# Performance work log

Hardware: AMD Instinct MI355X
Metric: run time of the kernel (lower is better)

Reference implementation:

```python
import jax, jax.numpy as jnp
import numpy as np

WD, WH, WW = 2, 7, 7
N = WD * WH * WW          # 98 tokens per window
DIM = 128
HEADS = 4
HEAD_DIM = DIM // HEADS   # 32
B_ = 2048                 # num_windows * batch
NW = 64                   # windows per image (mask leading dim)
TABLE = (2 * WD - 1) * (2 * WH - 1) * (2 * WW - 1)  # 507


def _relative_position_index():
    coords = np.stack(np.meshgrid(np.arange(WD), np.arange(WH), np.arange(WW), indexing='ij'))
    flat = coords.reshape(3, -1)                     # [3, N]
    rel = flat[:, :, None] - flat[:, None, :]        # [3, N, N]
    rel = rel.transpose(1, 2, 0).copy()              # [N, N, 3]
    rel[:, :, 0] += WD - 1
    rel[:, :, 1] += WH - 1
    rel[:, :, 2] += WW - 1
    rel[:, :, 0] *= (2 * WH - 1) * (2 * WW - 1)
    rel[:, :, 1] *= 2 * WW - 1
    return rel.sum(-1).astype(np.int32)             # [N, N]


def setup_inputs() -> dict:
    key = jax.random.key(0)
    ks = jax.random.split(key, 6)
    x = jax.random.normal(ks[0], (B_, N, DIM), dtype=jnp.float32)
    mask = jax.random.normal(ks[1], (NW, N, N), dtype=jnp.float32)
    qkv_w = jax.random.normal(ks[2], (3 * DIM, DIM), dtype=jnp.float32) * 0.02
    qkv_b = jnp.zeros((3 * DIM,), dtype=jnp.float32)
    proj_w = jax.random.normal(ks[3], (DIM, DIM), dtype=jnp.float32) * 0.02
    proj_b = jnp.zeros((DIM,), dtype=jnp.float32)
    bias_table = jax.random.normal(ks[4], (TABLE, HEADS), dtype=jnp.float32) * 0.02
    rel_idx = jnp.asarray(_relative_position_index())
    return {"x": x, "mask": mask, "qkv_w": qkv_w, "qkv_b": qkv_b,
            "proj_w": proj_w, "proj_b": proj_b, "bias_table": bias_table,
            "rel_idx": rel_idx}


def reference(x, mask, qkv_w, qkv_b, proj_w, proj_b, bias_table, rel_idx):
    b, n, c = x.shape
    hd = c // HEADS
    scale = hd ** -0.5
    qkv = x @ qkv_w.T + qkv_b                          # [B_, N, 3C]
    qkv = qkv.reshape(b, n, 3, HEADS, hd)
    qkv = jnp.transpose(qkv, (2, 0, 3, 1, 4))          # [3, B_, H, N, hd]
    q, k, v = qkv[0], qkv[1], qkv[2]
    attn = jnp.einsum('bhnd,bhmd->bhnm', q * scale, k)  # [B_, H, N, N]
    # gathered relative position bias
    bias = bias_table[rel_idx.reshape(-1)].reshape(n, n, HEADS)
    bias = jnp.transpose(bias, (2, 0, 1))               # [H, N, N]
    attn = attn + bias[None]
    nw = mask.shape[0]
    attn = attn.reshape(b // nw, nw, HEADS, n, n) + mask[None, :, None]
    attn = jax.nn.softmax(attn.reshape(b, HEADS, n, n), axis=-1)
    out = jnp.einsum('bhnm,bhmd->bnhd', attn, v).reshape(b, n, c)
    out = out @ proj_w.T + proj_b
    return out
```

## Files before the change

kernel.cpp:

```cpp
#include <hip/hip_runtime.h>
#include <stdint.h>

#define NTOK 98
#define DIM 128
#define HEADS 4
#define HD 32
#define BWIN 2048
#define NW 64
#define SCALE 0.17677669529663687f
#define QSTR 40
#define VSTR 104

typedef __bf16 bf16_t;
typedef bf16_t bf16x8 __attribute__((ext_vector_type(8)));
typedef float f32x4 __attribute__((ext_vector_type(4)));
typedef unsigned short u16;
typedef unsigned int u32;
typedef unsigned long long u64;

__device__ __forceinline__ u16 f2bf(float f) {
    union { bf16_t h; u16 u; } v; v.h = (bf16_t)f; return v.u;
}
__device__ __forceinline__ float bf2f(u16 b) {
    union { u16 u; bf16_t h; } v; v.u = b; return (float)v.h;
}

__global__ void k0_prep(const float* __restrict__ qkv_w, const float* __restrict__ proj_w,
                        const float* __restrict__ mask,
                        const float* __restrict__ bias_table, const int* __restrict__ rel_idx,
                        u16* __restrict__ qkvw_bf, u16* __restrict__ pw_bf,
                        u16* __restrict__ mbT)
{
    int t = blockIdx.x * 256 + threadIdx.x;
    if (t < 49152) {
        qkvw_bf[t] = f2bf(qkv_w[t]);
    } else if (t < 65536) {
        int r = t - 49152;
        pw_bf[r] = f2bf(proj_w[r]);
    } else {
        int r = t - 65536;
        int w    = r / 50176;
        int rem  = r - w * 50176;
        int hh   = rem / 12544;
        int rem2 = rem - hh * 12544;
        int i    = rem2 >> 7;
        int c    = rem2 & 127;
        int l16  = c >> 3;
        int njp  = c & 7;
        int j    = njp * 16 + l16;
        float val = 0.f;
        if (njp < 7 && j < NTOK)
            val = mask[w * 9604 + i * NTOK + j] + bias_table[rel_idx[i * NTOK + j] * HEADS + hh];
        mbT[r] = f2bf(val);
    }
}

__global__ __launch_bounds__(256, 4) void k_attn(
    const float* __restrict__ x, const u16* __restrict__ qkvw_bf,
    const float* __restrict__ qkv_b, const u16* __restrict__ mbT,
    u16* __restrict__ OG)
{
    __shared__ __align__(16) u16 qL[NTOK * QSTR];
    __shared__ __align__(16) u16 kL[NTOK * QSTR];
    __shared__ __align__(16) u16 vL[HD * VSTR];
    __shared__ __align__(16) u16 Pscr[4][16 * VSTR];

    const int bh   = (blockIdx.x & 7) * 1024 + (blockIdx.x >> 3);
    const int b    = bh >> 2;
    const int h    = bh & 3;
    const int tid  = threadIdx.x;
    const int wave = tid >> 6;
    const int lane = tid & 63;
    const int l16  = lane & 15;
    const int quad = lane >> 4;

    const float* xb = x + (size_t)b * (NTOK * DIM);

    {
        const int u0 = (wave * 21) >> 2;
        const int u1 = ((wave + 1) * 21) >> 2;
        int cached = -1;
        bf16x8 Bf[2][4];
        float  cb[2];
        for (int u = u0; u < u1; ++u) {
            const int part = u / 7;
            const int mt   = u - part * 7;
            if (part != cached) {
                const u16* wp = qkvw_bf + (size_t)part * DIM * DIM;
#pragma unroll
                for (int nt2 = 0; nt2 < 2; ++nt2) {
                    const int col = h * HD + nt2 * 16 + l16;
#pragma unroll
                    for (int ks = 0; ks < 4; ++ks)
                        Bf[nt2][ks] = *reinterpret_cast<const bf16x8*>(
                            wp + col * DIM + quad * 8 + ks * 32);
                    cb[nt2] = qkv_b[part * DIM + col];
                }
                cached = part;
            }
            int arow = mt * 16 + l16;
            if (arow > 97) arow = 97;
            bf16x8 af[4];
#pragma unroll
            for (int ks = 0; ks < 4; ++ks) {
                const float* xr = xb + arow * DIM + quad * 8 + ks * 32;
                const float4 a0 = *reinterpret_cast<const float4*>(xr);
                const float4 a1 = *reinterpret_cast<const float4*>(xr + 4);
                bf16x8 a;
                a[0] = (bf16_t)a0.x; a[1] = (bf16_t)a0.y; a[2] = (bf16_t)a0.z; a[3] = (bf16_t)a0.w;
                a[4] = (bf16_t)a1.x; a[5] = (bf16_t)a1.y; a[6] = (bf16_t)a1.z; a[7] = (bf16_t)a1.w;
                af[ks] = a;
            }
            f32x4 acc0 = {0.f, 0.f, 0.f, 0.f};
            f32x4 acc1 = {0.f, 0.f, 0.f, 0.f};
#pragma unroll
            for (int ks = 0; ks < 4; ++ks) {
                acc0 = __builtin_amdgcn_mfma_f32_16x16x32_bf16(af[ks], Bf[0][ks], acc0, 0, 0, 0);
                acc1 = __builtin_amdgcn_mfma_f32_16x16x32_bf16(af[ks], Bf[1][ks], acc1, 0, 0, 0);
            }
            const int tokb = mt * 16 + quad * 4;
#pragma unroll
            for (int nt2 = 0; nt2 < 2; ++nt2) {
                const f32x4& acc = nt2 ? acc1 : acc0;
                const int d = nt2 * 16 + l16;
                const float cbv = cb[nt2];
                if (part == 0) {
#pragma unroll
                    for (int reg = 0; reg < 4; ++reg) {
                        int tok = tokb + reg;
                        if (tok < NTOK)
                            qL[tok * QSTR + d] = f2bf((acc[reg] + cbv) * SCALE);
                    }
                } else if (part == 1) {
#pragma unroll
                    for (int reg = 0; reg < 4; ++reg) {
                        int tok = tokb + reg;
                        if (tok < NTOK)
                            kL[tok * QSTR + d] = f2bf(acc[reg] + cbv);
                    }
                } else {
                    u16* vrow = &vL[d * VSTR];
                    if (tokb + 3 <= 97) {
                        u64 pack = 0;
#pragma unroll
                        for (int reg = 0; reg < 4; ++reg)
                            pack |= ((u64)f2bf(acc[reg] + cbv)) << (16 * reg);
                        *reinterpret_cast<u64*>(&vrow[tokb]) = pack;
                    } else if (tokb <= 97) {
                        u32 pack = (u32)f2bf(acc[0] + cbv) | ((u32)f2bf(acc[1] + cbv) << 16);
                        *reinterpret_cast<u32*>(&vrow[tokb]) = pack;
                    }
                }
            }
        }
    }
    __syncthreads();

    {
        const u16* mbtp = mbT + ((size_t)((b & (NW - 1)) * HEADS + h)) * (NTOK * 128);
        u16* ps = &Pscr[wave][0];

        bf16x8 kf[7];
#pragma unroll
        for (int nj = 0; nj < 7; ++nj)
            kf[nj] = *reinterpret_cast<const bf16x8*>(&kL[(nj * 16 + l16) * QSTR + quad * 8]);

        for (int mi = 0; mi < 2; ++mi) {
            const int mt = wave + mi * 4;
            if (mt > 6) break;
            bf16x8 mrows[4];
#pragma unroll
            for (int reg = 0; reg < 4; ++reg) {
                int i  = mt * 16 + quad * 4 + reg;
                int ic = (i > 97) ? 97 : i;
                mrows[reg] = *reinterpret_cast<const bf16x8*>(&mbtp[ic * 128 + l16 * 8]);
            }
            bf16x8 qf = *reinterpret_cast<const bf16x8*>(&qL[(mt * 16 + l16) * QSTR + quad * 8]);
            f32x4 sacc[7];
#pragma unroll
            for (int nj = 0; nj < 7; ++nj) {
                f32x4 z = {0.f, 0.f, 0.f, 0.f};
                sacc[nj] = __builtin_amdgcn_mfma_f32_16x16x32_bf16(qf, kf[nj], z, 0, 0, 0);
            }
#pragma unroll
            for (int reg = 0; reg < 4; ++reg) {
                int i = mt * 16 + quad * 4 + reg;
                bool irow = (i < NTOK);
                float s[7];
#pragma unroll
                for (int nj = 0; nj < 7; ++nj) {
                    int j = nj * 16 + l16;
                    float val = -1e30f;
                    if (irow && j < NTOK)
                        val = sacc[nj][reg] + (float)mrows[reg][nj];
                    s[nj] = val;
                }
                float mx = s[0];
#pragma unroll
                for (int nj = 1; nj < 7; ++nj) mx = fmaxf(mx, s[nj]);
#pragma unroll
                for (int off = 1; off < 16; off <<= 1) mx = fmaxf(mx, __shfl_xor(mx, off));
                float p[7];
                float lsum = 0.f;
#pragma unroll
                for (int nj = 0; nj < 7; ++nj) {
                    float pv = (s[nj] > -1e29f) ? __expf(s[nj] - mx) : 0.f;
                    p[nj] = pv;
                    lsum += pv;
                }
#pragma unroll
                for (int off = 1; off < 16; off <<= 1) lsum += __shfl_xor(lsum, off);
                float rinv = 1.f / ((lsum > 0.f) ? lsum : 1.f);
#pragma unroll
                for (int nj = 0; nj < 7; ++nj) {
                    int j = nj * 16 + l16;
                    if (irow && j < NTOK)
                        ps[(quad * 4 + reg) * VSTR + j] = f2bf(p[nj] * rinv);
                }
            }
            bf16x8 pf[3];
#pragma unroll
            for (int ks = 0; ks < 3; ++ks)
                pf[ks] = *reinterpret_cast<const bf16x8*>(&ps[l16 * VSTR + quad * 8 + ks * 32]);
#pragma unroll
            for (int nt = 0; nt < 2; ++nt) {
                f32x4 oacc = {0.f, 0.f, 0.f, 0.f};
#pragma unroll
                for (int ks = 0; ks < 3; ++ks) {
                    bf16x8 vf = *reinterpret_cast<const bf16x8*>(
                        &vL[(nt * 16 + l16) * VSTR + quad * 8 + ks * 32]);
                    oacc = __builtin_amdgcn_mfma_f32_16x16x32_bf16(pf[ks], vf, oacc, 0, 0, 0);
                }
                int d = nt * 16 + l16;
                float v96 = bf2f(vL[d * VSTR + 96]);
                float v97 = bf2f(vL[d * VSTR + 97]);
#pragma unroll
                for (int reg = 0; reg < 4; ++reg) {
                    int i = mt * 16 + quad * 4 + reg;
                    if (i < NTOK) {
                        float p96 = bf2f(ps[(quad * 4 + reg) * VSTR + 96]);
                        float p97 = bf2f(ps[(quad * 4 + reg) * VSTR + 97]);
                        OG[((size_t)b * NTOK + i) * DIM + h * HD + d] =
                            f2bf(oacc[reg] + p96 * v96 + p97 * v97);
                    }
                }
            }
        }
    }
}

__global__ __launch_bounds__(256, 4) void k_proj(
    const u16* __restrict__ OG, const u16* __restrict__ pw_bf,
    const float* __restrict__ proj_b, float* __restrict__ out)
{
    const int b    = blockIdx.x;
    const int tid  = threadIdx.x;
    const int wave = tid >> 6;
    const int lane = tid & 63;
    const int l16  = lane & 15;
    const int quad = lane >> 4;

    bf16x8 bw[2][4];
    float  pb[2];
#pragma unroll
    for (int nt2 = 0; nt2 < 2; ++nt2) {
        const int col = (wave * 2 + nt2) * 16 + l16;
#pragma unroll
        for (int ks = 0; ks < 4; ++ks)
            bw[nt2][ks] = *reinterpret_cast<const bf16x8*>(
                pw_bf + col * DIM + quad * 8 + ks * 32);
        pb[nt2] = proj_b[col];
    }
    const u16* ob = OG + (size_t)b * (NTOK * DIM);
    for (int mt = 0; mt < 7; ++mt) {
        int arow = mt * 16 + l16;
        if (arow > 97) arow = 97;
        bf16x8 af[4];
#pragma unroll
        for (int ks = 0; ks < 4; ++ks)
            af[ks] = *reinterpret_cast<const bf16x8*>(ob + arow * DIM + quad * 8 + ks * 32);
        f32x4 acc0 = {0.f, 0.f, 0.f, 0.f};
        f32x4 acc1 = {0.f, 0.f, 0.f, 0.f};
#pragma unroll
        for (int ks = 0; ks < 4; ++ks) {
            acc0 = __builtin_amdgcn_mfma_f32_16x16x32_bf16(af[ks], bw[0][ks], acc0, 0, 0, 0);
            acc1 = __builtin_amdgcn_mfma_f32_16x16x32_bf16(af[ks], bw[1][ks], acc1, 0, 0, 0);
        }
#pragma unroll
        for (int nt2 = 0; nt2 < 2; ++nt2) {
            const f32x4& acc = nt2 ? acc1 : acc0;
            const int col = (wave * 2 + nt2) * 16 + l16;
#pragma unroll
            for (int reg = 0; reg < 4; ++reg) {
                int row = mt * 16 + quad * 4 + reg;
                if (row < NTOK)
                    out[((size_t)b * NTOK + row) * DIM + col] = acc[reg] + pb[nt2];
            }
        }
    }
}

extern "C" void kernel_launch(void* const* d_in, const int* in_sizes, int n_in,
                              void* d_out, int out_size, void* d_ws, size_t ws_size,
                              hipStream_t stream)
{
    const float* x       = (const float*)d_in[0];
    const float* mask    = (const float*)d_in[1];
    const float* qkv_w   = (const float*)d_in[2];
    const float* qkv_b   = (const float*)d_in[3];
    const float* proj_w  = (const float*)d_in[4];
    const float* proj_b  = (const float*)d_in[5];
    const float* bias_tb = (const float*)d_in[6];
    const int*   rel_idx = (const int*)d_in[7];
    float* out = (float*)d_out;

    char* ws = (char*)d_ws;
    u16* qkvw_bf = (u16*)(ws + 0);
    u16* pw_bf   = (u16*)(ws + 98304);
    u16* mbT     = (u16*)(ws + 131072);
    u16* OG      = (u16*)(ws + 6553600);

    k0_prep<<<12800, 256, 0, stream>>>(qkv_w, proj_w, mask, bias_tb, rel_idx,
                                       qkvw_bf, pw_bf, mbT);
    k_attn<<<BWIN * HEADS, 256, 0, stream>>>(x, qkvw_bf, qkv_b, mbT, OG);
    k_proj<<<BWIN, 256, 0, stream>>>(OG, pw_bf, proj_b, out);
}
```

Before: 389.4 us.

## Pre-convert x to bf16 in prep kernel and swizzle q/k LDS layout

The prep kernel now converts the fp32 input x to bf16 once, so each of the four per-head attention blocks loads bf16 directly instead of reloading fp32 and converting it. The q/k shared-memory stride shrinks from 40 to 32 and uses an XOR swizzle to avoid bank conflicts, which also frees LDS. Launch bounds are raised to target 5 blocks per CU. This adds an extra HBM write and read of x in bf16.

```diff
diff --git a/kernel.cpp b/kernel.cpp
--- a/kernel.cpp
+++ b/kernel.cpp
@@ -8,7 +8,7 @@
 #define BWIN 2048
 #define NW 64
 #define SCALE 0.17677669529663687f
-#define QSTR 40
+#define QSTR 32
 #define VSTR 104
 
 typedef __bf16 bf16_t;
@@ -24,12 +24,16 @@
 __device__ __forceinline__ float bf2f(u16 b) {
     union { u16 u; bf16_t h; } v; v.u = b; return (float)v.h;
 }
+__device__ __forceinline__ int qk_idx(int row, int d) {
+    return row * QSTR + ((((d >> 3) ^ (row & 3)) << 3) | (d & 7));
+}
 
 __global__ void k0_prep(const float* __restrict__ qkv_w, const float* __restrict__ proj_w,
                         const float* __restrict__ mask,
                         const float* __restrict__ bias_table, const int* __restrict__ rel_idx,
+                        const float* __restrict__ x,
                         u16* __restrict__ qkvw_bf, u16* __restrict__ pw_bf,
-                        u16* __restrict__ mbT)
+                        u16* __restrict__ mbT, u16* __restrict__ xbf)
 {
     int t = blockIdx.x * 256 + threadIdx.x;
     if (t < 49152) {
@@ -37,7 +41,7 @@
     } else if (t < 65536) {
         int r = t - 49152;
         pw_bf[r] = f2bf(proj_w[r]);
-    } else {
+    } else if (t < 3276800) {
         int r = t - 65536;
         int w    = r / 50176;
         int rem  = r - w * 50176;
@@ -52,11 +56,21 @@
         if (njp < 7 && j < NTOK)
             val = mask[w * 9604 + i * NTOK + j] + bias_table[rel_idx[i * NTOK + j] * HEADS + hh];
         mbT[r] = f2bf(val);
-    }
-}
-
-__global__ __launch_bounds__(256, 4) void k_attn(
-    const float* __restrict__ x, const u16* __restrict__ qkvw_bf,
+    } else if (t < 6488064) {
+        size_t idx = (size_t)(t - 3276800) * 8;
+        const float4 a0 = *reinterpret_cast<const float4*>(x + idx);
+        const float4 a1 = *reinterpret_cast<const float4*>(x + idx + 4);
+        u64 p0 = (u64)f2bf(a0.x) | ((u64)f2bf(a0.y) << 16) |
+                 ((u64)f2bf(a0.z) << 32) | ((u64)f2bf(a0.w) << 48);
+        u64 p1 = (u64)f2bf(a1.x) | ((u64)f2bf(a1.y) << 16) |
+                 ((u64)f2bf(a1.z) << 32) | ((u64)f2bf(a1.w) << 48);
+        *reinterpret_cast<u64*>(&xbf[idx])     = p0;
+        *reinterpret_cast<u64*>(&xbf[idx + 4]) = p1;
+    }
+}
+
+__global__ __launch_bounds__(256, 5) void k_attn(
+    const u16* __restrict__ xbf, const u16* __restrict__ qkvw_bf,
     const float* __restrict__ qkv_b, const u16* __restrict__ mbT,
     u16* __restrict__ OG)
 {
@@ -74,7 +88,7 @@
     const int l16  = lane & 15;
     const int quad = lane >> 4;
 
-    const float* xb = x + (size_t)b * (NTOK * DIM);
+    const u16* xb = xbf + (size_t)b * (NTOK * DIM);
 
     {
         const int u0 = (wave * 21) >> 2;
@@ -102,15 +116,9 @@
             if (arow > 97) arow = 97;
             bf16x8 af[4];
 #pragma unroll
-            for (int ks = 0; ks < 4; ++ks) {
-                const float* xr = xb + arow * DIM + quad * 8 + ks * 32;
-                const float4 a0 = *reinterpret_cast<const float4*>(xr);
-                const float4 a1 = *reinterpret_cast<const float4*>(xr + 4);
-                bf16x8 a;
-                a[0] = (bf16_t)a0.x; a[1] = (bf16_t)a0.y; a[2] = (bf16_t)a0.z; a[3] = (bf16_t)a0.w;
-                a[4] = (bf16_t)a1.x; a[5] = (bf16_t)a1.y; a[6] = (bf16_t)a1.z; a[7] = (bf16_t)a1.w;
-                af[ks] = a;
-            }
+            for (int ks = 0; ks < 4; ++ks)
+                af[ks] = *reinterpret_cast<const bf16x8*>(
+                    xb + arow * DIM + quad * 8 + ks * 32);
             f32x4 acc0 = {0.f, 0.f, 0.f, 0.f};
             f32x4 acc1 = {0.f, 0.f, 0.f, 0.f};
 #pragma unroll
@@ -129,14 +137,14 @@
                     for (int reg = 0; reg < 4; ++reg) {
                         int tok = tokb + reg;
                         if (tok < NTOK)
-                            qL[tok * QSTR + d] = f2bf((acc[reg] + cbv) * SCALE);
+                            qL[qk_idx(tok, d)] = f2bf((acc[reg] + cbv) * SCALE);
                     }
                 } else if (part == 1) {
 #pragma unroll
                     for (int reg = 0; reg < 4; ++reg) {
                         int tok = tokb + reg;
                         if (tok < NTOK)
-                            kL[tok * QSTR + d] = f2bf(acc[reg] + cbv);
+                            kL[qk_idx(tok, d)] = f2bf(acc[reg] + cbv);
                     }
                 } else {
                     u16* vrow = &vL[d * VSTR];
@@ -159,11 +167,12 @@
     {
         const u16* mbtp = mbT + ((size_t)((b & (NW - 1)) * HEADS + h)) * (NTOK * 128);
         u16* ps = &Pscr[wave][0];
+        const int qko = ((quad ^ (l16 & 3)) << 3);
 
         bf16x8 kf[7];
 #pragma unroll
         for (int nj = 0; nj < 7; ++nj)
-            kf[nj] = *reinterpret_cast<const bf16x8*>(&kL[(nj * 16 + l16) * QSTR + quad * 8]);
+            kf[nj] = *reinterpret_cast<const bf16x8*>(&kL[(nj * 16 + l16) * QSTR + qko]);
 
         for (int mi = 0; mi < 2; ++mi) {
             const int mt = wave + mi * 4;
@@ -175,7 +184,7 @@
                 int ic = (i > 97) ? 97 : i;
                 mrows[reg] = *reinterpret_cast<const bf16x8*>(&mbtp[ic * 128 + l16 * 8]);
             }
-            bf16x8 qf = *reinterpret_cast<const bf16x8*>(&qL[(mt * 16 + l16) * QSTR + quad * 8]);
+            bf16x8 qf = *reinterpret_cast<const bf16x8*>(&qL[(mt * 16 + l16) * QSTR + qko]);
             f32x4 sacc[7];
 #pragma unroll
             for (int nj = 0; nj < 7; ++nj) {
@@ -318,10 +327,11 @@
     u16* qkvw_bf = (u16*)(ws + 0);
     u16* pw_bf   = (u16*)(ws + 98304);
     u16* mbT     = (u16*)(ws + 131072);
-    u16* OG      = (u16*)(ws + 6553600);
-
-    k0_prep<<<12800, 256, 0, stream>>>(qkv_w, proj_w, mask, bias_tb, rel_idx,
-                                       qkvw_bf, pw_bf, mbT);
-    k_attn<<<BWIN * HEADS, 256, 0, stream>>>(x, qkvw_bf, qkv_b, mbT, OG);
+    u16* xbf     = (u16*)(ws + 6553600);
+    u16* OG      = (u16*)(ws + 57933824);
+
+    k0_prep<<<25344, 256, 0, stream>>>(qkv_w, proj_w, mask, bias_tb, rel_idx, x,
+                                       qkvw_bf, pw_bf, mbT, xbf);
+    k_attn<<<BWIN * HEADS, 256, 0, stream>>>(xbf, qkvw_bf, qkv_b, mbT, OG);
     k_proj<<<BWIN, 256, 0, stream>>>(OG, pw_bf, proj_b, out);
 }
```

After: 387.4 us. About the same (-0.5%).
